# Kernel tuning notes

Measured on AMD Instinct MI355X. Metric: run time of the kernel, lower is better.

The kernel has to match this reference:

```python
import jax, jax.numpy as jnp
import numpy as np

N = 100000      # n_heads + n_tails (entities)
E = 3200000     # nnz of sparse A_in (avg degree 32)
D = 128         # in_dim == out_dim
LAMDA = 0.5
ALPHA = 0.1
L_LAYER = 1
NEG_SLOPE = 0.01  # torch LeakyReLU default


def _leaky_relu(x):
    return jnp.where(x >= 0, x, NEG_SLOPE * x)


def setup_inputs() -> dict:
    key = jax.random.key(0)
    ks = jax.random.split(key, 10)
    ego = jax.random.normal(ks[0], (N, D), jnp.float32) * 0.1
    h0 = jax.random.normal(ks[1], (N, D), jnp.float32) * 0.1
    row = jax.random.randint(ks[2], (E,), 0, N)
    col = jax.random.randint(ks[3], (E,), 0, N)
    vals = jax.random.uniform(ks[4], (E,), jnp.float32) / 32.0  # ~normalized adjacency
    stdv = 1.0 / np.sqrt(D)
    weight = jax.random.uniform(ks[5], (D, D), jnp.float32, -stdv, stdv)
    w1 = jax.random.normal(ks[6], (D, D), jnp.float32) * (1.0 / np.sqrt(D))
    b1 = jnp.zeros((D,), jnp.float32)
    w2 = jax.random.normal(ks[7], (D, D), jnp.float32) * (1.0 / np.sqrt(D))
    b2 = jnp.zeros((D,), jnp.float32)
    return {"ego_embeddings": ego, "h0": h0, "vals": vals, "weight": weight,
            "w1": w1, "b1": b1, "w2": w2, "b2": b2, "row": row, "col": col}


def reference(ego_embeddings, h0, vals, weight, w1, b1, w2, b2, row, col):
    # SpMM: side = A_in @ ego  (COO gather-scale-scatter)
    side = jax.ops.segment_sum(vals[:, None] * ego_embeddings[col], row,
                               num_segments=N)  # (N, D)

    # residual_connection with use_residual=True
    beta = np.float32(np.log(LAMDA / L_LAYER + 1.0))
    identity_mapping = (1.0 - beta) + beta * weight  # (D, D)

    def resid(hi):
        return ((1.0 - ALPHA) * hi + ALPHA * h0) @ identity_mapping

    # bi-interaction: sum branch + elementwise-product branch
    sum_emb = _leaky_relu(resid(ego_embeddings + side) @ w1 + b1)
    bi_emb = _leaky_relu(resid(ego_embeddings * side) @ w2 + b2)
    # message_dropout is identity in eval mode
    return sum_emb + bi_emb
```

## Files before the change

### kernel.cpp

```cpp
#include <hip/hip_runtime.h>
#include <stdint.h>

#define D 128
#define BETA 0.40546510810816444f
#define TSTR 136

#define NWG  128
#define MAXB 256

#define NWG2 256
#define BROWS 256
#define MAXB2 512

typedef __bf16 bf16x8 __attribute__((ext_vector_type(8)));
typedef float f32x4 __attribute__((ext_vector_type(4)));

__device__ __forceinline__ uint16_t f2bf(float f) {
    union { float f; uint32_t i; } x; x.f = f;
    uint32_t r = (x.i + 0x7fffu + ((x.i >> 16) & 1u)) >> 16;
    return (uint16_t)r;
}
__device__ __forceinline__ float lo_f(uint32_t u) { return __uint_as_float(u << 16); }
__device__ __forceinline__ float hi_f(uint32_t u) { return __uint_as_float(u & 0xffff0000u); }
__device__ __forceinline__ uint32_t pack2(float x, float y) {
    return (uint32_t)f2bf(x) | ((uint32_t)f2bf(y) << 16);
}

__global__ void k_hist(const int* __restrict__ row, int* __restrict__ deg, int E, int N) {
    int e = blockIdx.x * blockDim.x + threadIdx.x;
    if (e < E) {
        int r = row[e]; r = min(max(r, 0), N - 1);
        atomicAdd(&deg[r], 1);
    }
}

__global__ void k_scan1(const int* __restrict__ deg, int* __restrict__ inc,
                        int* __restrict__ bsum, int n) {
    __shared__ int s[1024];
    int i = blockIdx.x * 1024 + threadIdx.x;
    int v = (i < n) ? deg[i] : 0;
    s[threadIdx.x] = v;
    __syncthreads();
    for (int d = 1; d < 1024; d <<= 1) {
        int t = (threadIdx.x >= (unsigned)d) ? s[threadIdx.x - d] : 0;
        __syncthreads();
        s[threadIdx.x] += t;
        __syncthreads();
    }
    if (i < n) inc[i] = s[threadIdx.x];
    if (threadIdx.x == 1023) bsum[blockIdx.x] = s[1023];
}

__global__ void k_scan2(const int* __restrict__ bsum, int* __restrict__ boff,
                        int nb, int* __restrict__ rowptr, int N) {
    int run = 0;
    for (int b = 0; b < nb; b++) { boff[b] = run; run += bsum[b]; }
    rowptr[N] = run;
}

__global__ void k_scan3(const int* __restrict__ deg, const int* __restrict__ boff,
                        int* __restrict__ rowptr, int* __restrict__ wp, int n) {
    int i = blockIdx.x * 1024 + threadIdx.x;
    if (i < n) {
        int ex = rowptr[i] - deg[i] + boff[blockIdx.x];
        rowptr[i] = ex;
        wp[i] = ex;
    }
}

__global__ void k_scatter(const int* __restrict__ row, const int* __restrict__ col,
                          const float* __restrict__ vals, int* __restrict__ wp,
                          uint2* __restrict__ rec, int E, int N) {
    int e = blockIdx.x * blockDim.x + threadIdx.x;
    if (e < E) {
        int r = row[e]; r = min(max(r, 0), N - 1);
        int pos = atomicAdd(&wp[r], 1);
        pos = min(max(pos, 0), E - 1);
        uint2 rv;
        rv.x = (uint32_t)col[e];
        rv.y = __float_as_uint(vals[e]);
        rec[pos] = rv;
    }
}

__global__ void k_cvt(const float4* __restrict__ src, uint2* __restrict__ dst, int n) {
    int i = blockIdx.x * blockDim.x + threadIdx.x;
    if (i < n) {
        float4 v = src[i];
        uint2 o; o.x = pack2(v.x, v.y); o.y = pack2(v.z, v.w);
        dst[i] = o;
    }
}

__global__ void k_prep(const float* __restrict__ W, const float* __restrict__ w1,
                       const float* __restrict__ w2, uint16_t* __restrict__ M1T,
                       uint16_t* __restrict__ M2T) {
    int k = blockIdx.x, n = threadIdx.x;
    __shared__ float imrow[D];
    imrow[n] = (1.0f - BETA) + BETA * W[k * D + n];
    __syncthreads();
    float s1 = 0.f, s2 = 0.f;
    for (int j = 0; j < D; j++) {
        float im = imrow[j];
        s1 += im * w1[j * D + n];
        s2 += im * w2[j * D + n];
    }
    M1T[n * D + k] = f2bf(s1);
    M2T[n * D + k] = f2bf(s2);
}

__global__ __launch_bounds__(256) void k_front(
        const float* __restrict__ W, const float* __restrict__ w1,
        const float* __restrict__ w2, uint16_t* __restrict__ M1T,
        uint16_t* __restrict__ M2T,
        const float4* __restrict__ egoq, uint2* __restrict__ egobq, int nquads,
        const int* __restrict__ row, int* __restrict__ cnt,
        int E, int N, int nbuck, int cvtB) {
    __shared__ int h[MAXB2];
    __shared__ float imrow[2][D];
    int tid = threadIdx.x;
    int bid = blockIdx.x;

    if (bid < 64) {
        int half = tid >> 7;
        int n = tid & 127;
        int k = bid * 2 + half;
        imrow[half][n] = (1.0f - BETA) + BETA * W[k * D + n];
        __syncthreads();
        float s1 = 0.f, s2 = 0.f;
        for (int j = 0; j < D; j++) {
            float im = imrow[half][j];
            s1 += im * w1[j * D + n];
            s2 += im * w2[j * D + n];
        }
        M1T[n * D + k] = f2bf(s1);
        M2T[n * D + k] = f2bf(s2);
        return;
    }
    if (bid < 64 + cvtB) {
        int i = (bid - 64) * 256 + tid;
        if (i < nquads) {
            float4 v = egoq[i];
            uint2 o; o.x = pack2(v.x, v.y); o.y = pack2(v.z, v.w);
            egobq[i] = o;
        }
        return;
    }
    int w = bid - 64 - cvtB;
    for (int b = tid; b < nbuck; b += 256) h[b] = 0;
    __syncthreads();
    int chunk = (E + NWG2 - 1) / NWG2;
    int beg = w * chunk, end = min(beg + chunk, E);
    for (int e = beg + tid; e < end; e += 256) {
        int r = row[e]; r = min(max(r, 0), N - 1);
        atomicAdd(&h[r >> 8], 1);
    }
    __syncthreads();
    for (int b = tid; b < nbuck; b += 256) cnt[b * NWG2 + w] = h[b];
}

__global__ __launch_bounds__(512) void k_group2(const int* __restrict__ row,
                                                const int* __restrict__ col,
                                                const float* __restrict__ vals,
                                                const int* __restrict__ cnt,
                                                int* __restrict__ bbase,
                                                uint2* __restrict__ grouped,
                                                int E, int N, int nbuck) {
    __shared__ int s[512];
    __shared__ int bb[MAXB2 + 1];
    __shared__ int lbase[MAXB2];
    __shared__ int lcnt[MAXB2];
    int t = threadIdx.x;
    int w = blockIdx.x;

    int tot = 0;
    if (t < nbuck) {
        const int4* p4 = (const int4*)(cnt + t * NWG2);
#pragma unroll 4
        for (int i2 = 0; i2 < NWG2 / 4; i2++) {
            int4 v = p4[i2];
            tot += v.x + v.y + v.z + v.w;
        }
    }
    s[t] = tot;
    __syncthreads();
    for (int d = 1; d < 512; d <<= 1) {
        int x = (t >= d) ? s[t - d] : 0;
        __syncthreads();
        s[t] += x;
        __syncthreads();
    }
    if (t < nbuck) bb[t] = s[t] - tot;
    if (t == 511) bb[nbuck] = s[511];
    __syncthreads();
    if (w == 0) {
        for (int b = t; b <= nbuck; b += 512) bbase[b] = bb[b];
    }

    for (int b = t; b < nbuck; b += 512) {
        const int* cr = cnt + b * NWG2;
        int off = bb[b];
        for (int w2 = 0; w2 < w; w2++) off += cr[w2];
        lbase[b] = off;
        lcnt[b] = 0;
    }
    __syncthreads();
    int chunk = (E + NWG2 - 1) / NWG2;
    int beg = w * chunk, end = min(beg + chunk, E);
    for (int e = beg + t; e < end; e += 512) {
        int r = row[e]; r = min(max(r, 0), N - 1);
        int c = col[e]; c = min(max(c, 0), N - 1);
        int b = r >> 8;
        int lp = atomicAdd(&lcnt[b], 1);
        int pos = lbase[b] + lp;
        pos = min(max(pos, 0), E - 1);
        uint2 g;
        g.x = ((uint32_t)(r & 255) << 17) | (uint32_t)c;
        g.y = __float_as_uint(vals[e]);
        grouped[pos] = g;
    }
}

__global__ __launch_bounds__(512) void k_place2(const uint2* __restrict__ grouped,
                                                const int* __restrict__ bbase,
                                                int* __restrict__ rowptr,
                                                uint2* __restrict__ rec,
                                                int E, int N, int nbuck) {
    __shared__ int lh[BROWS];
    __shared__ int lcc[BROWS];
    __shared__ int ps[BROWS];
    int b = blockIdx.x;
    int t = threadIdx.x;
    int pb = bbase[b], pe = bbase[b + 1];
    if (t < BROWS) { lh[t] = 0; lcc[t] = 0; }
    __syncthreads();
    for (int i = pb + t; i < pe; i += 512)
        atomicAdd(&lh[grouped[i].x >> 17], 1);
    __syncthreads();
    int v = (t < BROWS) ? lh[t] : 0;
    if (t < BROWS) ps[t] = v;
    __syncthreads();
    for (int d = 1; d < BROWS; d <<= 1) {
        int x = (t < BROWS && t >= d) ? ps[t - d] : 0;
        __syncthreads();
        if (t < BROWS) ps[t] += x;
        __syncthreads();
    }
    if (t < BROWS) lh[t] = ps[t] - v;
    __syncthreads();
    int rbase = b << 8;
    if (t < BROWS) {
        int r = rbase + t;
        if (r < N) rowptr[r] = pb + lh[t];
    }
    if (b == nbuck - 1 && t == 0) rowptr[N] = E;
    for (int i = pb + t; i < pe; i += 512) {
        uint2 g = grouped[i];
        int rl = (int)(g.x >> 17);
        int lp = atomicAdd(&lcc[rl], 1);
        int pos = pb + lh[rl] + lp;
        pos = min(max(pos, 0), E - 1);
        uint2 rv; rv.x = g.x & 0x1FFFFu; rv.y = g.y;
        rec[pos] = rv;
    }
}

__device__ __forceinline__ void gemm_phase(
        const uint16_t* sT1, const uint16_t* sT2,
        const uint16_t* __restrict__ M1T, const uint16_t* __restrict__ M2T,
        const float* __restrict__ b1, const float* __restrict__ b2,
        float* __restrict__ out, int base, int wave, int lane, int N) {
    int l15 = lane & 15, quad = lane >> 4;
#pragma unroll
    for (int t = 0; t < 2; t++) {
        int tn = wave * 2 + t;
        f32x4 acc1 = {0.f, 0.f, 0.f, 0.f}, acc2 = {0.f, 0.f, 0.f, 0.f};
#pragma unroll
        for (int kb = 0; kb < 4; kb++) {
            int ko = kb * 32 + quad * 8;
            bf16x8 a1 = *(const bf16x8*)(sT1 + l15 * TSTR + ko);
            bf16x8 a2 = *(const bf16x8*)(sT2 + l15 * TSTR + ko);
            bf16x8 bb1 = *(const bf16x8*)(M1T + (tn * 16 + l15) * D + ko);
            bf16x8 bb2 = *(const bf16x8*)(M2T + (tn * 16 + l15) * D + ko);
            acc1 = __builtin_amdgcn_mfma_f32_16x16x32_bf16(a1, bb1, acc1, 0, 0, 0);
            acc2 = __builtin_amdgcn_mfma_f32_16x16x32_bf16(a2, bb2, acc2, 0, 0, 0);
        }
        int colo = tn * 16 + l15;
        float bbias1 = b1[colo], bbias2 = b2[colo];
#pragma unroll
        for (int r = 0; r < 4; r++) {
            int rowi = base + quad * 4 + r;
            if (rowi < N) {
                float v1 = acc1[r] + bbias1;
                v1 = (v1 >= 0.f) ? v1 : 0.01f * v1;
                float v2 = acc2[r] + bbias2;
                v2 = (v2 >= 0.f) ? v2 : 0.01f * v2;
                out[(size_t)rowi * D + colo] = v1 + v2;
            }
        }
    }
}

__global__ __launch_bounds__(256) void k_fused(
        const int* __restrict__ rowptr, const uint2* __restrict__ rec,
        const uint32_t* __restrict__ egob,
        const float2* __restrict__ egf, const float2* __restrict__ hh,
        const uint16_t* __restrict__ M1T, const uint16_t* __restrict__ M2T,
        const float* __restrict__ b1, const float* __restrict__ b2,
        float* __restrict__ out, int N) {
    __shared__ __attribute__((aligned(16))) uint16_t sT1[16 * TSTR];
    __shared__ __attribute__((aligned(16))) uint16_t sT2[16 * TSTR];
    int tid = threadIdx.x;
    int wave = tid >> 6, lane = tid & 63;
    int base = blockIdx.x * 16;
    uint32_t* s1d = (uint32_t*)sT1;
    uint32_t* s2d = (uint32_t*)sT2;

#pragma unroll
    for (int i = 0; i < 4; i++) {
        int node = __builtin_amdgcn_readfirstlane(base + wave * 4 + i);
        float t1x = 0.f, t1y = 0.f, t2x = 0.f, t2y = 0.f;
        if (node < N) {
            int e0 = rowptr[node], e1 = rowptr[node + 1];
            float ax = 0.f, ay = 0.f, bx = 0.f, by = 0.f;
            int e = e0;
            for (; e + 8 <= e1; e += 8) {
                uint2 r0 = rec[e + 0], r1 = rec[e + 1], r2 = rec[e + 2], r3 = rec[e + 3];
                uint2 r4 = rec[e + 4], r5 = rec[e + 5], r6 = rec[e + 6], r7 = rec[e + 7];
                int c0 = min(max((int)r0.x, 0), N - 1);
                int c1 = min(max((int)r1.x, 0), N - 1);
                int c2 = min(max((int)r2.x, 0), N - 1);
                int c3 = min(max((int)r3.x, 0), N - 1);
                int c4 = min(max((int)r4.x, 0), N - 1);
                int c5 = min(max((int)r5.x, 0), N - 1);
                int c6 = min(max((int)r6.x, 0), N - 1);
                int c7 = min(max((int)r7.x, 0), N - 1);
                uint32_t u0 = egob[c0 * 64 + lane];
                uint32_t u1 = egob[c1 * 64 + lane];
                uint32_t u2 = egob[c2 * 64 + lane];
                uint32_t u3 = egob[c3 * 64 + lane];
                uint32_t u4 = egob[c4 * 64 + lane];
                uint32_t u5 = egob[c5 * 64 + lane];
                uint32_t u6 = egob[c6 * 64 + lane];
                uint32_t u7 = egob[c7 * 64 + lane];
                float v0 = __uint_as_float(r0.y), v1 = __uint_as_float(r1.y);
                float v2 = __uint_as_float(r2.y), v3 = __uint_as_float(r3.y);
                float v4 = __uint_as_float(r4.y), v5 = __uint_as_float(r5.y);
                float v6 = __uint_as_float(r6.y), v7 = __uint_as_float(r7.y);
                ax += v0 * lo_f(u0); ay += v0 * hi_f(u0);
                bx += v1 * lo_f(u1); by += v1 * hi_f(u1);
                ax += v2 * lo_f(u2); ay += v2 * hi_f(u2);
                bx += v3 * lo_f(u3); by += v3 * hi_f(u3);
                ax += v4 * lo_f(u4); ay += v4 * hi_f(u4);
                bx += v5 * lo_f(u5); by += v5 * hi_f(u5);
                ax += v6 * lo_f(u6); ay += v6 * hi_f(u6);
                bx += v7 * lo_f(u7); by += v7 * hi_f(u7);
            }
            if (e < e1) {
                int last = e1 - 1;
                uint2 rr[8];
#pragma unroll
                for (int k = 0; k < 8; k++) {
                    int idx = e + k;
                    rr[k] = rec[(idx <= last) ? idx : last];
                }
                uint32_t uu[8];
#pragma unroll
                for (int k = 0; k < 8; k++) {
                    int c = min(max((int)rr[k].x, 0), N - 1);
                    uu[k] = egob[c * 64 + lane];
                }
#pragma unroll
                for (int k = 0; k < 8; k++) {
                    float v = (e + k < e1) ? __uint_as_float(rr[k].y) : 0.f;
                    if (k & 1) { bx += v * lo_f(uu[k]); by += v * hi_f(uu[k]); }
                    else       { ax += v * lo_f(uu[k]); ay += v * hi_f(uu[k]); }
                }
            }
            ax += bx; ay += by;
            float2 se = egf[node * 64 + lane];
            float2 sh = hh[node * 64 + lane];
            t1x = 0.9f * (se.x + ax) + 0.1f * sh.x;
            t1y = 0.9f * (se.y + ay) + 0.1f * sh.y;
            t2x = 0.9f * (se.x * ax) + 0.1f * sh.x;
            t2y = 0.9f * (se.y * ay) + 0.1f * sh.y;
        }
        int r = wave * 4 + i;
        s1d[r * (TSTR / 2) + lane] = pack2(t1x, t1y);
        s2d[r * (TSTR / 2) + lane] = pack2(t2x, t2y);
    }
    __syncthreads();
    gemm_phase(sT1, sT2, M1T, M2T, b1, b2, out, base, wave, lane, N);
}

__global__ __launch_bounds__(256) void k_coo_side(
        const int* __restrict__ row, const int* __restrict__ col,
        const float* __restrict__ vals, const float2* __restrict__ egf,
        float* __restrict__ sideF, int E, int N) {
    long long t = (long long)blockIdx.x * blockDim.x + threadIdx.x;
    int e = (int)(t >> 6), l = (int)(t & 63);
    if (e >= E) return;
    int c = col[e]; c = min(max(c, 0), N - 1);
    int r = row[e]; r = min(max(r, 0), N - 1);
    float v = vals[e];
    float2 u = egf[c * 64 + l];
    atomicAdd(&sideF[r * D + 2 * l],     v * u.x);
    atomicAdd(&sideF[r * D + 2 * l + 1], v * u.y);
}

__global__ __launch_bounds__(256) void k_fused2(
        const float2* __restrict__ egf, const float2* __restrict__ hh,
        const uint16_t* __restrict__ M1T, const uint16_t* __restrict__ M2T,
        const float* __restrict__ b1, const float* __restrict__ b2,
        float* __restrict__ out, int N) {
    __shared__ __attribute__((aligned(16))) uint16_t sT1[16 * TSTR];
    __shared__ __attribute__((aligned(16))) uint16_t sT2[16 * TSTR];
    int tid = threadIdx.x;
    int wave = tid >> 6, lane = tid & 63;
    int base = blockIdx.x * 16;
    const float2* sd = (const float2*)out;
    uint32_t* s1d = (uint32_t*)sT1;
    uint32_t* s2d = (uint32_t*)sT2;

#pragma unroll
    for (int i = 0; i < 4; i++) {
        int node = base + wave * 4 + i;
        float t1x = 0.f, t1y = 0.f, t2x = 0.f, t2y = 0.f;
        if (node < N) {
            float2 us = sd[node * 64 + lane];
            float2 se = egf[node * 64 + lane];
            float2 sh = hh[node * 64 + lane];
            t1x = 0.9f * (se.x + us.x) + 0.1f * sh.x;
            t1y = 0.9f * (se.y + us.y) + 0.1f * sh.y;
            t2x = 0.9f * (se.x * us.x) + 0.1f * sh.x;
            t2y = 0.9f * (se.y * us.y) + 0.1f * sh.y;
        }
        int r = wave * 4 + i;
        s1d[r * (TSTR / 2) + lane] = pack2(t1x, t1y);
        s2d[r * (TSTR / 2) + lane] = pack2(t2x, t2y);
    }
    __syncthreads();
    gemm_phase(sT1, sT2, M1T, M2T, b1, b2, out, base, wave, lane, N);
}

extern "C" void kernel_launch(void* const* d_in, const int* in_sizes, int n_in,
                              void* d_out, int out_size, void* d_ws, size_t ws_size,
                              hipStream_t stream) {
    const float* ego  = (const float*)d_in[0];
    const float* h0   = (const float*)d_in[1];
    const float* vals = (const float*)d_in[2];
    const float* W    = (const float*)d_in[3];
    const float* w1   = (const float*)d_in[4];
    const float* b1   = (const float*)d_in[5];
    const float* w2   = (const float*)d_in[6];
    const float* b2   = (const float*)d_in[7];
    const int* row = (const int*)d_in[8];
    const int* col = (const int*)d_in[9];
    int N = in_sizes[0] / D;
    int E = in_sizes[2];

    int nbuck2 = (N + 255) >> 8;
    size_t cnt_elems = (size_t)nbuck2 * NWG2 + 2;
    if (cnt_elems < (size_t)MAXB * NWG + 1) cnt_elems = (size_t)MAXB * NWG + 1;

    char* p = (char*)d_ws;
    auto alloc = [&](size_t bytes) -> char* {
        char* q = p;
        p += (bytes + 511) & ~(size_t)511;
        return q;
    };
    uint16_t* M1T    = (uint16_t*)alloc(D * D * 2);
    uint16_t* M2T    = (uint16_t*)alloc(D * D * 2);
    uint32_t* egob   = (uint32_t*)alloc((size_t)N * 64 * 4);
    int*      deg    = (int*)alloc((size_t)N * 4);
    int*      rowptr = (int*)alloc((size_t)(N + 1) * 4);
    int*      wp     = (int*)alloc((size_t)N * 4);
    int*      bsum   = (int*)alloc(1024 * 4);
    int*      boff   = (int*)alloc(1024 * 4);
    int*      cnt    = (int*)alloc(cnt_elems * 4);
    uint2*    rec    = (uint2*)alloc((size_t)E * 8);
    size_t need_fast = (size_t)(p - (char*)d_ws);

    if (ws_size >= need_fast) {
        int nquads = N * 32;
        bool bucket_ok = (nbuck2 <= MAXB2) && ((size_t)out_size * 4 >= (size_t)E * 8);
        if (bucket_ok) {
            int cvtB = (nquads + 255) / 256;
            k_front<<<64 + cvtB + NWG2, 256, 0, stream>>>(
                W, w1, w2, M1T, M2T,
                (const float4*)ego, (uint2*)egob, nquads,
                row, cnt, E, N, nbuck2, cvtB);
            k_group2<<<NWG2, 512, 0, stream>>>(row, col, vals, cnt, boff,
                                               (uint2*)d_out, E, N, nbuck2);
            k_place2<<<nbuck2, 512, 0, stream>>>((const uint2*)d_out, boff,
                                                 rowptr, rec, E, N, nbuck2);
        } else {
            k_prep<<<D, D, 0, stream>>>(W, w1, w2, M1T, M2T);
            k_cvt<<<(nquads + 255) / 256, 256, 0, stream>>>((const float4*)ego,
                                                            (uint2*)egob, nquads);
            hipMemsetAsync(deg, 0, (size_t)N * 4, stream);
            int nb = (N + 1023) / 1024;
            k_hist<<<(E + 255) / 256, 256, 0, stream>>>(row, deg, E, N);
            k_scan1<<<nb, 1024, 0, stream>>>(deg, rowptr, bsum, N);
            k_scan2<<<1, 1, 0, stream>>>(bsum, boff, nb, rowptr, N);
            k_scan3<<<nb, 1024, 0, stream>>>(deg, boff, rowptr, wp, N);
            k_scatter<<<(E + 255) / 256, 256, 0, stream>>>(row, col, vals, wp,
                                                           rec, E, N);
        }
        int nblocks = (N + 15) / 16;
        k_fused<<<nblocks, 256, 0, stream>>>(rowptr, rec, egob,
                                             (const float2*)ego, (const float2*)h0,
                                             M1T, M2T, b1, b2, (float*)d_out, N);
    } else {
        k_prep<<<D, D, 0, stream>>>(W, w1, w2, M1T, M2T);
        hipMemsetAsync(d_out, 0, (size_t)out_size * 4, stream);
        long long tthr = (long long)E * 64;
        int blocks = (int)((tthr + 255) / 256);
        k_coo_side<<<blocks, 256, 0, stream>>>(row, col, vals, (const float2*)ego,
                                               (float*)d_out, E, N);
        int nblocks = (N + 15) / 16;
        k_fused2<<<nblocks, 256, 0, stream>>>((const float2*)ego, (const float2*)h0,
                                              M1T, M2T, b1, b2, (float*)d_out, N);
    }
}
```

Baseline: 448.9 us.

## Interleave two nodes' gathers in fused SpMM and halve the sort bucket size

The fused SpMM-GEMM kernel now walks the edge lists of two adjacent nodes together in 8-edge steps. This keeps more independent gather loads in flight per wave, hiding latency. The row-bucketing sort now uses 128-row buckets instead of 256, which doubles the bucket count and the number of k_place2 blocks, so each scan thread in k_group2 handles two buckets. The trade-off is more register pressure in the fused kernel, imbalance when two nodes' degrees differ, and extra scan work.

Measured after the change: 485.6 us. 1.08x slower.

```diff
diff --git a/kernel.cpp b/kernel.cpp
--- a/kernel.cpp
+++ b/kernel.cpp
@@ -9,8 +9,9 @@
 #define MAXB 256
 
 #define NWG2 256
-#define BROWS 256
-#define MAXB2 512
+#define BROWS 128
+#define BSH   7
+#define MAXB2 1024
 
 typedef __bf16 bf16x8 __attribute__((ext_vector_type(8)));
 typedef float f32x4 __attribute__((ext_vector_type(4)));
@@ -153,7 +154,7 @@
     int beg = w * chunk, end = min(beg + chunk, E);
     for (int e = beg + tid; e < end; e += 256) {
         int r = row[e]; r = min(max(r, 0), N - 1);
-        atomicAdd(&h[r >> 8], 1);
+        atomicAdd(&h[r >> BSH], 1);
     }
     __syncthreads();
     for (int b = tid; b < nbuck; b += 256) cnt[b * NWG2 + w] = h[b];
@@ -173,16 +174,25 @@
     int t = threadIdx.x;
     int w = blockIdx.x;
 
-    int tot = 0;
-    if (t < nbuck) {
-        const int4* p4 = (const int4*)(cnt + t * NWG2);
+    int t0 = 2 * t, t1v = 2 * t + 1;
+    int totA = 0, totB = 0;
+    if (t0 < nbuck) {
+        const int4* p4 = (const int4*)(cnt + t0 * NWG2);
 #pragma unroll 4
         for (int i2 = 0; i2 < NWG2 / 4; i2++) {
             int4 v = p4[i2];
-            tot += v.x + v.y + v.z + v.w;
-        }
-    }
-    s[t] = tot;
+            totA += v.x + v.y + v.z + v.w;
+        }
+    }
+    if (t1v < nbuck) {
+        const int4* p4 = (const int4*)(cnt + t1v * NWG2);
+#pragma unroll 4
+        for (int i2 = 0; i2 < NWG2 / 4; i2++) {
+            int4 v = p4[i2];
+            totB += v.x + v.y + v.z + v.w;
+        }
+    }
+    s[t] = totA + totB;
     __syncthreads();
     for (int d = 1; d < 512; d <<= 1) {
         int x = (t >= d) ? s[t - d] : 0;
@@ -190,7 +200,9 @@
         s[t] += x;
         __syncthreads();
     }
-    if (t < nbuck) bb[t] = s[t] - tot;
+    int ex = s[t] - (totA + totB);
+    if (t0 < nbuck) bb[t0] = ex;
+    if (t1v < nbuck) bb[t1v] = ex + totA;
     if (t == 511) bb[nbuck] = s[511];
     __syncthreads();
     if (w == 0) {
@@ -210,12 +222,12 @@
     for (int e = beg + t; e < end; e += 512) {
         int r = row[e]; r = min(max(r, 0), N - 1);
         int c = col[e]; c = min(max(c, 0), N - 1);
-        int b = r >> 8;
+        int b = r >> BSH;
         int lp = atomicAdd(&lcnt[b], 1);
         int pos = lbase[b] + lp;
         pos = min(max(pos, 0), E - 1);
         uint2 g;
-        g.x = ((uint32_t)(r & 255) << 17) | (uint32_t)c;
+        g.x = ((uint32_t)(r & (BROWS - 1)) << 17) | (uint32_t)c;
         g.y = __float_as_uint(vals[e]);
         grouped[pos] = g;
     }
@@ -248,7 +260,7 @@
     }
     if (t < BROWS) lh[t] = ps[t] - v;
     __syncthreads();
-    int rbase = b << 8;
+    int rbase = b << BSH;
     if (t < BROWS) {
         int r = rbase + t;
         if (r < N) rowptr[r] = pb + lh[t];
@@ -298,6 +310,32 @@
                 out[(size_t)rowi * D + colo] = v1 + v2;
             }
         }
+    }
+}
+
+template<bool MASKED>
+__device__ __forceinline__ void step8(const uint2* __restrict__ rec,
+                                      const uint32_t* __restrict__ egob,
+                                      int lane, int N, int e, int e1,
+                                      float& ax, float& ay) {
+    int last = e1 - 1;
+    uint2 rr[8];
+#pragma unroll
+    for (int k = 0; k < 8; k++) {
+        int idx = MASKED ? ((e + k <= last) ? e + k : last) : (e + k);
+        rr[k] = rec[idx];
+    }
+    uint32_t uu[8];
+#pragma unroll
+    for (int k = 0; k < 8; k++) {
+        int c = min(max((int)rr[k].x, 0), N - 1);
+        uu[k] = egob[c * 64 + lane];
+    }
+#pragma unroll
+    for (int k = 0; k < 8; k++) {
+        float v = (!MASKED || (e + k < e1)) ? __uint_as_float(rr[k].y) : 0.f;
+        ax += v * lo_f(uu[k]);
+        ay += v * hi_f(uu[k]);
     }
 }
 
@@ -317,77 +355,57 @@
     uint32_t* s2d = (uint32_t*)sT2;
 
 #pragma unroll
-    for (int i = 0; i < 4; i++) {
-        int node = __builtin_amdgcn_readfirstlane(base + wave * 4 + i);
-        float t1x = 0.f, t1y = 0.f, t2x = 0.f, t2y = 0.f;
-        if (node < N) {
-            int e0 = rowptr[node], e1 = rowptr[node + 1];
-            float ax = 0.f, ay = 0.f, bx = 0.f, by = 0.f;
-            int e = e0;
-            for (; e + 8 <= e1; e += 8) {
-                uint2 r0 = rec[e + 0], r1 = rec[e + 1], r2 = rec[e + 2], r3 = rec[e + 3];
-                uint2 r4 = rec[e + 4], r5 = rec[e + 5], r6 = rec[e + 6], r7 = rec[e + 7];
-                int c0 = min(max((int)r0.x, 0), N - 1);
-                int c1 = min(max((int)r1.x, 0), N - 1);
-                int c2 = min(max((int)r2.x, 0), N - 1);
-                int c3 = min(max((int)r3.x, 0), N - 1);
-                int c4 = min(max((int)r4.x, 0), N - 1);
-                int c5 = min(max((int)r5.x, 0), N - 1);
-                int c6 = min(max((int)r6.x, 0), N - 1);
-                int c7 = min(max((int)r7.x, 0), N - 1);
-                uint32_t u0 = egob[c0 * 64 + lane];
-                uint32_t u1 = egob[c1 * 64 + lane];
-                uint32_t u2 = egob[c2 * 64 + lane];
-                uint32_t u3 = egob[c3 * 64 + lane];
-                uint32_t u4 = egob[c4 * 64 + lane];
-                uint32_t u5 = egob[c5 * 64 + lane];
-                uint32_t u6 = egob[c6 * 64 + lane];
-                uint32_t u7 = egob[c7 * 64 + lane];
-                float v0 = __uint_as_float(r0.y), v1 = __uint_as_float(r1.y);
-                float v2 = __uint_as_float(r2.y), v3 = __uint_as_float(r3.y);
-                float v4 = __uint_as_float(r4.y), v5 = __uint_as_float(r5.y);
-                float v6 = __uint_as_float(r6.y), v7 = __uint_as_float(r7.y);
-                ax += v0 * lo_f(u0); ay += v0 * hi_f(u0);
-                bx += v1 * lo_f(u1); by += v1 * hi_f(u1);
-                ax += v2 * lo_f(u2); ay += v2 * hi_f(u2);
-                bx += v3 * lo_f(u3); by += v3 * hi_f(u3);
-                ax += v4 * lo_f(u4); ay += v4 * hi_f(u4);
-                bx += v5 * lo_f(u5); by += v5 * hi_f(u5);
-                ax += v6 * lo_f(u6); ay += v6 * hi_f(u6);
-                bx += v7 * lo_f(u7); by += v7 * hi_f(u7);
+    for (int pi = 0; pi < 2; pi++) {
+        int nodeA = __builtin_amdgcn_readfirstlane(base + wave * 4 + pi * 2);
+        int nodeB = nodeA + 1;
+        int a0 = 0, a1 = 0, b0 = 0, b1e = 0;
+        if (nodeA < N) {
+            a0 = rowptr[nodeA];
+            a1 = rowptr[nodeA + 1];
+            if (nodeB < N) { b0 = a1; b1e = rowptr[nodeB + 1]; }
+        }
+        float axA = 0.f, ayA = 0.f, axB = 0.f, ayB = 0.f;
+        int eA = a0, eB = b0;
+        for (; eA + 8 <= a1 && eB + 8 <= b1e; eA += 8, eB += 8) {
+            step8<false>(rec, egob, lane, N, eA, a1, axA, ayA);
+            step8<false>(rec, egob, lane, N, eB, b1e, axB, ayB);
+        }
+        for (; eA + 8 <= a1; eA += 8)
+            step8<false>(rec, egob, lane, N, eA, a1, axA, ayA);
+        if (eA < a1)
+            step8<true>(rec, egob, lane, N, eA, a1, axA, ayA);
+        for (; eB + 8 <= b1e; eB += 8)
+            step8<false>(rec, egob, lane, N, eB, b1e, axB, ayB);
+        if (eB < b1e)
+            step8<true>(rec, egob, lane, N, eB, b1e, axB, ayB);
+        {
+            float t1x = 0.f, t1y = 0.f, t2x = 0.f, t2y = 0.f;
+            if (nodeA < N) {
+                float2 se = egf[nodeA * 64 + lane];
+                float2 sh = hh[nodeA * 64 + lane];
+                t1x = 0.9f * (se.x + axA) + 0.1f * sh.x;
+                t1y = 0.9f * (se.y + ayA) + 0.1f * sh.y;
+                t2x = 0.9f * (se.x * axA) + 0.1f * sh.x;
+                t2y = 0.9f * (se.y * ayA) + 0.1f * sh.y;
             }
-            if (e < e1) {
-                int last = e1 - 1;
-                uint2 rr[8];
-#pragma unroll
-                for (int k = 0; k < 8; k++) {
-                    int idx = e + k;
-                    rr[k] = rec[(idx <= last) ? idx : last];
-                }
-                uint32_t uu[8];
-#pragma unroll
-                for (int k = 0; k < 8; k++) {
-                    int c = min(max((int)rr[k].x, 0), N - 1);
-                    uu[k] = egob[c * 64 + lane];
-                }
-#pragma unroll
-                for (int k = 0; k < 8; k++) {
-                    float v = (e + k < e1) ? __uint_as_float(rr[k].y) : 0.f;
-                    if (k & 1) { bx += v * lo_f(uu[k]); by += v * hi_f(uu[k]); }
-                    else       { ax += v * lo_f(uu[k]); ay += v * hi_f(uu[k]); }
-                }
+            int r = wave * 4 + pi * 2;
+            s1d[r * (TSTR / 2) + lane] = pack2(t1x, t1y);
+            s2d[r * (TSTR / 2) + lane] = pack2(t2x, t2y);
+        }
+        {
+            float t1x = 0.f, t1y = 0.f, t2x = 0.f, t2y = 0.f;
+            if (nodeB < N) {
+                float2 se = egf[nodeB * 64 + lane];
+                float2 sh = hh[nodeB * 64 + lane];
+                t1x = 0.9f * (se.x + axB) + 0.1f * sh.x;
+                t1y = 0.9f * (se.y + ayB) + 0.1f * sh.y;
+                t2x = 0.9f * (se.x * axB) + 0.1f * sh.x;
+                t2y = 0.9f * (se.y * ayB) + 0.1f * sh.y;
             }
-            ax += bx; ay += by;
-            float2 se = egf[node * 64 + lane];
-            float2 sh = hh[node * 64 + lane];
-            t1x = 0.9f * (se.x + ax) + 0.1f * sh.x;
-            t1y = 0.9f * (se.y + ay) + 0.1f * sh.y;
-            t2x = 0.9f * (se.x * ax) + 0.1f * sh.x;
-            t2y = 0.9f * (se.y * ay) + 0.1f * sh.y;
-        }
-        int r = wave * 4 + i;
-        s1d[r * (TSTR / 2) + lane] = pack2(t1x, t1y);
-        s2d[r * (TSTR / 2) + lane] = pack2(t2x, t2y);
+            int r = wave * 4 + pi * 2 + 1;
+            s1d[r * (TSTR / 2) + lane] = pack2(t1x, t1y);
+            s2d[r * (TSTR / 2) + lane] = pack2(t2x, t2y);
+        }
     }
     __syncthreads();
     gemm_phase(sT1, sT2, M1T, M2T, b1, b2, out, base, wave, lane, N);
@@ -459,7 +477,7 @@
     int N = in_sizes[0] / D;
     int E = in_sizes[2];
 
-    int nbuck2 = (N + 255) >> 8;
+    int nbuck2 = (N + BROWS - 1) >> BSH;
     size_t cnt_elems = (size_t)nbuck2 * NWG2 + 2;
     if (cnt_elems < (size_t)MAXB * NWG + 1) cnt_elems = (size_t)MAXB * NWG + 1;
 
@@ -476,7 +494,7 @@
     int*      rowptr = (int*)alloc((size_t)(N + 1) * 4);
     int*      wp     = (int*)alloc((size_t)N * 4);
     int*      bsum   = (int*)alloc(1024 * 4);
-    int*      boff   = (int*)alloc(1024 * 4);
+    int*      boff   = (int*)alloc((MAXB2 + 2) * 4);
     int*      cnt    = (int*)alloc(cnt_elems * 4);
     uint2*    rec    = (uint2*)alloc((size_t)E * 8);
     size_t need_fast = (size_t)(p - (char*)d_ws);
```
